# Kernel optimization log

Measured on AMD Instinct MI355X. Metric: run time of the kernel, lower is better.

## Reference

```python
import math
import jax, jax.numpy as jnp
import numpy as np

EMBED_DIM = 2048
NUM_HEADS = 16
NUM_KV_HEADS = 8
DEPTH = 12
HEAD_DIM = EMBED_DIM // NUM_HEADS // 2  # 64
N_REP = NUM_HEADS // NUM_KV_HEADS       # 2
SCALING = HEAD_DIM ** (-0.5)
LAMBDA_INIT = 0.8 - 0.6 * math.exp(-0.3 * DEPTH)
EPS = 1e-5


def _rope_cos_sin(seq_len, head_dim, offset=0):
    pos = jnp.arange(offset, offset + seq_len, dtype=jnp.float32)
    theta = jnp.arange(0, head_dim, 2, dtype=jnp.float32) / head_dim
    inv_freq = 1.0 / (10000.0 ** theta + 1e-8)
    sinusoid = pos[:, None] * inv_freq[None, :]  # [seq, head_dim//2]
    return jnp.cos(sinusoid), jnp.sin(sinusoid)


def _apply_rotary_interleaved(x, cos, sin):
    # x: [b, s, h, d]; cos/sin: [s, d//2]; interleaved pairs (even, odd)
    x1 = x[..., 0::2]
    x2 = x[..., 1::2]
    c = cos[None, :, None, :]
    s = sin[None, :, None, :]
    o1 = x1 * c - x2 * s
    o2 = x1 * s + x2 * c
    return jnp.stack([o1, o2], axis=-1).reshape(x.shape)


def setup_inputs() -> dict:
    key = jax.random.key(0)
    ks = jax.random.split(key, 12)
    d = EMBED_DIM
    inp = {
        "q": jax.random.normal(ks[0], (1, 2048, d), dtype=jnp.float32),
        "k": jax.random.normal(ks[1], (1, 2048, d), dtype=jnp.float32),
        "v": jax.random.normal(ks[2], (1, 2048, d), dtype=jnp.float32),
        "Wq": jax.random.normal(ks[3], (d, d), dtype=jnp.float32) * (d ** -0.5),
        "Wk": jax.random.normal(ks[4], (d, d // N_REP), dtype=jnp.float32) * (d ** -0.5),
        "Wv": jax.random.normal(ks[5], (d, d // N_REP), dtype=jnp.float32) * (d ** -0.5),
        "Wout": jax.random.normal(ks[6], (d, d), dtype=jnp.float32) * (d ** -0.5),
        "lq1": jax.random.normal(ks[7], (HEAD_DIM,), dtype=jnp.float32) * 0.1,
        "lk1": jax.random.normal(ks[8], (HEAD_DIM,), dtype=jnp.float32) * 0.1,
        "lq2": jax.random.normal(ks[9], (HEAD_DIM,), dtype=jnp.float32) * 0.1,
        "lk2": jax.random.normal(ks[10], (HEAD_DIM,), dtype=jnp.float32) * 0.1,
        "subln_w": jnp.ones((2 * HEAD_DIM,), dtype=jnp.float32),
    }
    return inp


def reference(q, k, v, Wq, Wk, Wv, Wout, lq1, lk1, lq2, lk2, subln_w):
    bsz, tgt_len, _ = q.shape
    src_len = k.shape[1]
    hd = HEAD_DIM

    qp = (q @ Wq).reshape(bsz, tgt_len, 2 * NUM_HEADS, hd)
    kp = (k @ Wk).reshape(bsz, src_len, 2 * NUM_KV_HEADS, hd)
    vp = (v @ Wv).reshape(bsz, src_len, NUM_KV_HEADS, 2 * hd)

    q_cos, q_sin = _rope_cos_sin(tgt_len, hd)
    k_cos, k_sin = _rope_cos_sin(src_len, hd)
    qp = _apply_rotary_interleaved(qp, q_cos, q_sin)
    kp = _apply_rotary_interleaved(kp, k_cos, k_sin)

    qp = jnp.transpose(qp, (0, 2, 1, 3)) * SCALING          # [b, 2H, t, hd]
    kp = jnp.repeat(jnp.transpose(kp, (0, 2, 1, 3)), N_REP, axis=1)  # [b, 2H, s, hd]
    vp = jnp.repeat(jnp.transpose(vp, (0, 2, 1, 3)), N_REP, axis=1)  # [b, H, s, 2hd]

    attn_weights = jnp.einsum('bhtd,bhsd->bhts', qp, kp)
    attn_weights = jax.nn.softmax(attn_weights.astype(jnp.float32), axis=-1).astype(qp.dtype)

    lambda_1 = jnp.exp(jnp.sum(lq1 * lk1))
    lambda_2 = jnp.exp(jnp.sum(lq2 * lk2))
    lambda_full = lambda_1 - lambda_2 + LAMBDA_INIT

    attn_weights = attn_weights.reshape(bsz, NUM_HEADS, 2, tgt_len, src_len)
    attn_weights = attn_weights[:, :, 0] - lambda_full * attn_weights[:, :, 1]

    attn = jnp.einsum('bhts,bhsd->bhtd', attn_weights, vp)  # [b, H, t, 2hd]

    # RMSNorm over last dim with affine weight
    rms = jax.lax.rsqrt(jnp.mean(jnp.square(attn), axis=-1, keepdims=True) + EPS)
    attn = attn * rms * subln_w
    attn = attn * (1.0 - LAMBDA_INIT)

    attn = jnp.transpose(attn, (0, 2, 1, 3)).reshape(bsz, tgt_len, NUM_HEADS * 2 * hd)
    return attn @ Wout
```

## Files before the change

### kernel.cpp

```cpp
#include <hip/hip_runtime.h>

typedef unsigned short u16;
typedef unsigned int u32;
typedef float f32x4 __attribute__((ext_vector_type(4)));
typedef __bf16 bf16x8 __attribute__((ext_vector_type(8)));
typedef __bf16 bf16x4 __attribute__((ext_vector_type(4)));

#define LAMBDA_INIT_F 0.7836057665316245f
#define ONE_MINUS_LI  0.2163942334683755f
#define THR_LOG2 11.0f
#define Q_SCALE 0.18033688011112042f

__device__ __forceinline__ u16 f2b(float f) {
  union { float f; u32 u; } x; x.f = f;
  u32 r = x.u + 0x7fffu + ((x.u >> 16) & 1u);
  return (u16)(r >> 16);
}

__device__ __forceinline__ f32x4 mfma16(bf16x8 a, bf16x8 b, f32x4 c) {
  return __builtin_amdgcn_mfma_f32_16x16x32_bf16(a, b, c, 0, 0, 0);
}

__device__ __forceinline__ float fexp2(float x) { return __builtin_amdgcn_exp2f(x); }

__device__ __forceinline__ void gll16(const void* gp, void* lp) {
  __builtin_amdgcn_global_load_lds((__attribute__((address_space(1))) void*)(gp),
                                   (__attribute__((address_space(3))) void*)(lp),
                                   16, 0, 0);
}

__global__ __launch_bounds__(256) void cast3_kernel(const float* __restrict__ q,
                                                    const float* __restrict__ k,
                                                    const float* __restrict__ v,
                                                    u16* __restrict__ qb,
                                                    u16* __restrict__ kb,
                                                    u16* __restrict__ vb) {
  int bid = blockIdx.x;
  int seg = bid >> 11;
  int i = (bid & 2047) * 256 + threadIdx.x;
  const float* in = seg == 0 ? q : (seg == 1 ? k : v);
  u16* out = seg == 0 ? qb : (seg == 1 ? kb : vb);
  const f32x4* p = (const f32x4*)(in + (size_t)i * 8);
  f32x4 a = p[0], b = p[1];
  union { u16 u[8]; f32x4 v; } o;
#pragma unroll
  for (int j = 0; j < 4; ++j) { o.u[j] = f2b(a[j]); o.u[4 + j] = f2b(b[j]); }
  *(f32x4*)(out + (size_t)i * 8) = o.v;
}

__device__ __forceinline__ void trans_body(const float* __restrict__ in,
                                           u16* __restrict__ out, int R, int C) {
  __shared__ float tile[32][33];
  int bx = blockIdx.x * 32;
  int by = blockIdx.y * 32;
  int tx = threadIdx.x & 31, ty = threadIdx.x >> 5;
#pragma unroll
  for (int i = 0; i < 32; i += 8)
    tile[ty + i][tx] = in[(size_t)(by + ty + i) * C + bx + tx];
  __syncthreads();
#pragma unroll
  for (int i = 0; i < 32; i += 8)
    out[(size_t)(bx + ty + i) * R + by + tx] = f2b(tile[tx][ty + i]);
}

__global__ __launch_bounds__(256) void wtrans_kernel(
    const float* __restrict__ Wq, u16* __restrict__ WqT,
    const float* __restrict__ Wk, u16* __restrict__ WkT,
    const float* __restrict__ Wv, u16* __restrict__ WvT,
    const float* __restrict__ Wo, u16* __restrict__ WoT) {
  int z = blockIdx.z;
  const float* in;
  u16* out;
  int C;
  if (z == 0)      { in = Wq; out = WqT; C = 2048; }
  else if (z == 1) { in = Wk; out = WkT; C = 1024; }
  else if (z == 2) { in = Wv; out = WvT; C = 1024; }
  else             { in = Wo; out = WoT; C = 2048; }
  if (blockIdx.x * 32 >= C) return;
  trans_body(in, out, 2048, C);
}

__global__ __launch_bounds__(256) void vtrans_kernel(const float* __restrict__ in,
                                                     u16* __restrict__ out) {
  __shared__ float tile[32][33];
  int bx = blockIdx.x * 32;
  int by = blockIdx.y * 32;
  int tx = threadIdx.x & 31, ty = threadIdx.x >> 5;
#pragma unroll
  for (int i = 0; i < 32; i += 8)
    tile[ty + i][tx] = in[(size_t)(by + ty + i) * 1024 + bx + tx];
  __syncthreads();
  int ptx = 8 * ((tx >> 2) & 3) + 4 * (tx >> 4) + (tx & 3);
#pragma unroll
  for (int i = 0; i < 32; i += 8)
    out[(size_t)(bx + ty + i) * 2048 + by + ptx] = f2b(tile[tx][ty + i]);
}

__global__ __launch_bounds__(256) void rope2_kernel(const float* __restrict__ QP,
                                                    const float* __restrict__ KP,
                                                    u16* __restrict__ Qh,
                                                    u16* __restrict__ Kh) {
  int hh = blockIdx.y;
  int idx = blockIdx.x * 256 + threadIdx.x;
  int j = idx & 31;
  int t = idx >> 5;
  const float* in;
  u16* out;
  int Hh, hl;
  float scale;
  if (hh < 32) { in = QP; out = Qh; Hh = 32; hl = hh; scale = Q_SCALE; }
  else         { in = KP; out = Kh; Hh = 16; hl = hh - 32; scale = 1.0f; }
  const float* src = in + (size_t)t * (Hh * 64) + hl * 64 + 2 * j;
  float x1 = src[0], x2 = src[1];
  float theta = (float)j * (1.0f / 32.0f);
  float denom = expf(theta * 9.210340371976184f);
  float invf = 1.0f / (denom + 1e-8f);
  float ang = (float)t * invf;
  float s = sinf(ang), c = cosf(ang);
  float o1 = (x1 * c - x2 * s) * scale;
  float o2 = (x1 * s + x2 * c) * scale;
  u32 pk = (u32)f2b(o1) | ((u32)f2b(o2) << 16);
  *(u32*)(out + ((size_t)hl * 2048 + t) * 64 + 2 * j) = pk;
}

__device__ __forceinline__ void gemm_body64(u16* As, u16* Bs,
                                            const u16* __restrict__ A,
                                            const u16* __restrict__ Bt,
                                            float* __restrict__ C,
                                            int N, int K, int bx, int by) {
  const int tid = threadIdx.x;
  const int lane = tid & 63;
  const int wave = tid >> 6;
  const int m0 = by * 128;
  const int n0 = bx * 64;
  const int wm = (wave >> 1) * 64;
  const int wn = (wave & 1) * 32;
  const int g = lane >> 4, c = lane & 15;

  f32x4 acc[4][2];
#pragma unroll
  for (int i = 0; i < 4; ++i)
#pragma unroll
    for (int j = 0; j < 2; ++j) acc[i][j] = (f32x4){0.f, 0.f, 0.f, 0.f};

  for (int k0 = 0; k0 < K; k0 += 64) {
    __syncthreads();
#pragma unroll
    for (int it = 0; it < 4; ++it) {
      int gi = it * 256 + tid;
      int R = gi >> 3;
      int lg = (gi & 7) ^ (R & 7);
      gll16(A + (size_t)(m0 + R) * K + k0 + lg * 8, As + gi * 8);
    }
#pragma unroll
    for (int it = 0; it < 2; ++it) {
      int gi = it * 256 + tid;
      int R = gi >> 3;
      int lg = (gi & 7) ^ (R & 7);
      gll16(Bt + (size_t)(n0 + R) * K + k0 + lg * 8, Bs + gi * 8);
    }
    __syncthreads();
#pragma unroll
    for (int kk = 0; kk < 2; ++kk) {
      bf16x8 af[4], bf[2];
      int ph = ((kk * 4 + g) ^ (c & 7)) * 8;
#pragma unroll
      for (int i = 0; i < 4; ++i) af[i] = *(const bf16x8*)&As[(wm + i * 16 + c) * 64 + ph];
#pragma unroll
      for (int j = 0; j < 2; ++j) bf[j] = *(const bf16x8*)&Bs[(wn + j * 16 + c) * 64 + ph];
#pragma unroll
      for (int i = 0; i < 4; ++i)
#pragma unroll
        for (int j = 0; j < 2; ++j) acc[i][j] = mfma16(af[i], bf[j], acc[i][j]);
    }
  }
#pragma unroll
  for (int i = 0; i < 4; ++i)
#pragma unroll
    for (int j = 0; j < 2; ++j) {
      int mrow = m0 + wm + i * 16 + g * 4;
      int ncol = n0 + wn + j * 16 + c;
#pragma unroll
      for (int r = 0; r < 4; ++r) C[(size_t)(mrow + r) * N + ncol] = acc[i][j][r];
    }
}

__global__ __launch_bounds__(256, 4) void gemm_qkv_kernel(
    const u16* __restrict__ qb, const u16* __restrict__ WqT, float* __restrict__ QP,
    const u16* __restrict__ kb, const u16* __restrict__ WkT, float* __restrict__ KP,
    const u16* __restrict__ vb, const u16* __restrict__ WvT, float* __restrict__ VP) {
  __shared__ u16 As[128 * 64];
  __shared__ u16 Bs[64 * 64];
  int bid = ((blockIdx.x & 7) << 7) | (blockIdx.x >> 3);
  if (bid < 512) {
    gemm_body64(As, Bs, qb, WqT, QP, 2048, 2048, bid & 31, bid >> 5);
  } else if (bid < 768) {
    int t = bid - 512;
    gemm_body64(As, Bs, kb, WkT, KP, 1024, 2048, t & 15, t >> 4);
  } else {
    int t = bid - 768;
    gemm_body64(As, Bs, vb, WvT, VP, 1024, 2048, t & 15, t >> 4);
  }
}

__global__ __launch_bounds__(256, 2) void gemm_one_kernel(const u16* __restrict__ A,
                                                          const u16* __restrict__ Bt,
                                                          float* __restrict__ C) {
  __shared__ u16 As[128 * 64];
  __shared__ u16 Bs[64 * 64];
  int bid = ((blockIdx.x & 7) << 6) | (blockIdx.x >> 3);
  gemm_body64(As, Bs, A, Bt, C, 2048, 2048, bid & 31, bid >> 5);
}

__global__ __launch_bounds__(512, 2) void attn_kernel(const u16* __restrict__ Qb,
                                                      const u16* __restrict__ Kb,
                                                      const u16* __restrict__ Vt,
                                                      u16* __restrict__ AO,
                                                      const float* __restrict__ lq1,
                                                      const float* __restrict__ lk1,
                                                      const float* __restrict__ lq2,
                                                      const float* __restrict__ lk2,
                                                      const float* __restrict__ subln) {
  const int b = ((blockIdx.x & 7) << 5) | (blockIdx.x >> 3);
  const int h = b >> 4;
  const int tid = threadIdx.x;
  const int wave = tid >> 6;
  const int lane = tid & 63;
  const int t0 = ((b & 15) * 8 + wave) * 16;
  const int g = lane >> 4, c = lane & 15;
  const int c7 = c & 7;

  __shared__ u16 smem[24576];

  const u16* Kh = Kb + (size_t)h * 2048 * 64;
  const u16* Vh = Vt + (size_t)(h >> 1) * 128 * 2048;

  float myl1 = lq1[lane] * lk1[lane];
  float myl2 = lq2[lane] * lk2[lane];
#pragma unroll
  for (int off = 32; off; off >>= 1) {
    myl1 += __shfl_xor(myl1, off);
    myl2 += __shfl_xor(myl2, off);
  }
  const float lambda_full = expf(myl1) - expf(myl2) + LAMBDA_INIT_F;

  bf16x8 qf[2][2];
#pragma unroll
  for (int e = 0; e < 2; ++e)
#pragma unroll
    for (int d = 0; d < 2; ++d)
      qf[e][d] = *(const bf16x8*)(Qb + ((size_t)(2 * h + e) * 2048 + t0 + c) * 64 + d * 32 + g * 8);

  const int kb0 = c * 64 + ((g ^ c7) * 8);
  const int kb1 = kb0 ^ 32;

  const u16* ksrc0;
  const u16* vsrc0;
  const u16* vsrc1;
  { int gi = tid;       int R = gi >> 3; ksrc0 = Kh + R * 64 + ((gi & 7) ^ (R & 7)) * 8; }
  { int gi = tid;       int R = gi >> 3; vsrc0 = Vh + (size_t)R * 2048 + ((gi & 7) ^ (R & 7)) * 8; }
  { int gi = 512 + tid; int R = gi >> 3; vsrc1 = Vh + (size_t)R * 2048 + ((gi & 7) ^ (R & 7)) * 8; }

  f32x4 O[2][8];
#pragma unroll
  for (int e = 0; e < 2; ++e)
#pragma unroll
    for (int f = 0; f < 8; ++f) O[e][f] = (f32x4){0.f, 0.f, 0.f, 0.f};
  float m0 = -1e30f, m1 = -1e30f, ls0 = 0.f, ls1 = 0.f;

#define STAGE(kOff, vOff, s0)                                   \
  do {                                                          \
    gll16(ksrc0 + (size_t)(s0) * 64, smem + (kOff) + tid * 8);  \
    gll16(vsrc0 + (s0), smem + (vOff) + tid * 8);               \
    gll16(vsrc1 + (s0), smem + (vOff) + 4096 + tid * 8);        \
  } while (0)

#define TILE(kOff, vOff)                                                      \
  do {                                                                        \
    bf16x8 kf[4][2];                                                          \
    _Pragma("unroll") for (int sf = 0; sf < 4; ++sf) {                        \
      kf[sf][0] = *(const bf16x8*)&smem[(kOff) + kb0 + sf * 1024];            \
      kf[sf][1] = *(const bf16x8*)&smem[(kOff) + kb1 + sf * 1024];            \
    }                                                                         \
    f32x4 sa[2][4];                                                           \
    _Pragma("unroll") for (int e = 0; e < 2; ++e)                             \
      _Pragma("unroll") for (int sf = 0; sf < 4; ++sf) {                      \
        f32x4 z = (f32x4){0.f, 0.f, 0.f, 0.f};                                \
        z = mfma16(kf[sf][0], qf[e][0], z);                                   \
        z = mfma16(kf[sf][1], qf[e][1], z);                                   \
        sa[e][sf] = z;                                                        \
      }                                                                       \
    bf16x8 vv0[8];                                                            \
    _Pragma("unroll") for (int f = 0; f < 8; ++f)                             \
      vv0[f] = *(const bf16x8*)&smem[(vOff) + kb0 + f * 1024];                \
    bf16x8 paf[2][2];                                                         \
    _Pragma("unroll") for (int e = 0; e < 2; ++e) {                           \
      float& m_e = e ? m1 : m0;                                               \
      float& ls_e = e ? ls1 : ls0;                                            \
      float mx = sa[e][0][0];                                                 \
      _Pragma("unroll") for (int sf = 0; sf < 4; ++sf)                        \
        _Pragma("unroll") for (int r = 0; r < 4; ++r)                         \
          mx = fmaxf(mx, sa[e][sf][r]);                                       \
      mx = fmaxf(mx, __shfl_xor(mx, 16));                                     \
      mx = fmaxf(mx, __shfl_xor(mx, 32));                                     \
      if (__any(mx > m_e + THR_LOG2)) {                                       \
        float mn = fmaxf(m_e, mx);                                            \
        float sc = fexp2(m_e - mn);                                           \
        m_e = mn;                                                             \
        ls_e *= sc;                                                           \
        float scr[4];                                                         \
        _Pragma("unroll") for (int r = 0; r < 4; ++r) scr[r] = __shfl(sc, g * 4 + r); \
        _Pragma("unroll") for (int ff = 0; ff < 8; ++ff)                      \
          _Pragma("unroll") for (int r = 0; r < 4; ++r) O[e][ff][r] *= scr[r]; \
      }                                                                       \
      float p[4][4];                                                          \
      float sum = 0.f;                                                        \
      _Pragma("unroll") for (int sf = 0; sf < 4; ++sf)                        \
        _Pragma("unroll") for (int r = 0; r < 4; ++r) {                       \
          float pv = fexp2(sa[e][sf][r] - m_e);                               \
          p[sf][r] = pv;                                                      \
          sum += pv;                                                          \
        }                                                                     \
      sum += __shfl_xor(sum, 16);                                             \
      sum += __shfl_xor(sum, 32);                                             \
      ls_e += sum;                                                            \
      paf[e][0] = (bf16x8){(__bf16)p[0][0], (__bf16)p[0][1], (__bf16)p[0][2], (__bf16)p[0][3], \
                           (__bf16)p[1][0], (__bf16)p[1][1], (__bf16)p[1][2], (__bf16)p[1][3]}; \
      paf[e][1] = (bf16x8){(__bf16)p[2][0], (__bf16)p[2][1], (__bf16)p[2][2], (__bf16)p[2][3], \
                           (__bf16)p[3][0], (__bf16)p[3][1], (__bf16)p[3][2], (__bf16)p[3][3]}; \
    }                                                                         \
    __builtin_amdgcn_s_setprio(1);                                            \
    bf16x8 vv1[8];                                                            \
    _Pragma("unroll") for (int f = 0; f < 8; ++f)                             \
      vv1[f] = *(const bf16x8*)&smem[(vOff) + kb1 + f * 1024];                \
    _Pragma("unroll") for (int f = 0; f < 8; ++f) {                           \
      O[0][f] = mfma16(paf[0][0], vv0[f], O[0][f]);                           \
      O[1][f] = mfma16(paf[1][0], vv0[f], O[1][f]);                           \
    }                                                                         \
    _Pragma("unroll") for (int f = 0; f < 8; ++f) {                           \
      O[0][f] = mfma16(paf[0][1], vv1[f], O[0][f]);                           \
      O[1][f] = mfma16(paf[1][1], vv1[f], O[1][f]);                           \
    }                                                                         \
    __builtin_amdgcn_s_setprio(0);                                            \
  } while (0)

  STAGE(0, 8192, 0);

#pragma unroll 1
  for (int t = 0; t < 32; t += 2) {
    __syncthreads();
    STAGE(4096, 16384, (t + 1) * 64);
    TILE(0, 8192);
    __syncthreads();
    if (t < 30) STAGE(0, 8192, (t + 2) * 64);
    TILE(4096, 16384);
  }

  float inv0 = 1.f / ls0, inv1 = 1.f / ls1;
  float i0[4], i1[4];
#pragma unroll
  for (int r = 0; r < 4; ++r) {
    i0[r] = __shfl(inv0, g * 4 + r);
    i1[r] = __shfl(inv1, g * 4 + r);
  }
  float res[8][4];
  float ss[4] = {0.f, 0.f, 0.f, 0.f};
#pragma unroll
  for (int f = 0; f < 8; ++f)
#pragma unroll
    for (int r = 0; r < 4; ++r) {
      float vv = O[0][f][r] * i0[r] - lambda_full * (O[1][f][r] * i1[r]);
      res[f][r] = vv;
      ss[r] += vv * vv;
    }
#pragma unroll
  for (int off = 1; off < 16; off <<= 1)
#pragma unroll
    for (int r = 0; r < 4; ++r) ss[r] += __shfl_xor(ss[r], off);
  float rms[4];
#pragma unroll
  for (int r = 0; r < 4; ++r)
    rms[r] = rsqrtf(ss[r] * (1.0f / 128.0f) + 1e-5f) * ONE_MINUS_LI;
  float w[8];
#pragma unroll
  for (int f = 0; f < 8; ++f) w[f] = subln[f * 16 + c];
#pragma unroll
  for (int f = 0; f < 8; ++f)
#pragma unroll
    for (int r = 0; r < 4; ++r)
      AO[(size_t)(t0 + g * 4 + r) * 2048 + h * 128 + f * 16 + c] = f2b(res[f][r] * rms[r] * w[f]);
}

extern "C" void kernel_launch(void* const* d_in, const int* in_sizes, int n_in,
                              void* d_out, int out_size, void* d_ws, size_t ws_size,
                              hipStream_t stream) {
  const float* q     = (const float*)d_in[0];
  const float* k     = (const float*)d_in[1];
  const float* v     = (const float*)d_in[2];
  const float* Wq    = (const float*)d_in[3];
  const float* Wk    = (const float*)d_in[4];
  const float* Wv    = (const float*)d_in[5];
  const float* Wout  = (const float*)d_in[6];
  const float* lq1   = (const float*)d_in[7];
  const float* lk1   = (const float*)d_in[8];
  const float* lq2   = (const float*)d_in[9];
  const float* lk2   = (const float*)d_in[10];
  const float* subln = (const float*)d_in[11];
  float* out = (float*)d_out;

  char* ws = (char*)d_ws;
  size_t off = 0;
  auto alloc = [&](size_t bytes) -> void* {
    void* p = ws + off;
    off += (bytes + 255) & ~(size_t)255;
    return p;
  };
  u16* qb  = (u16*)alloc(2048ull * 2048 * 2);
  u16* kb  = (u16*)alloc(2048ull * 2048 * 2);
  u16* vb  = (u16*)alloc(2048ull * 2048 * 2);
  u16* WqT = (u16*)alloc(2048ull * 2048 * 2);
  u16* WkT = (u16*)alloc(1024ull * 2048 * 2);
  u16* WvT = (u16*)alloc(1024ull * 2048 * 2);
  u16* WoT = (u16*)alloc(2048ull * 2048 * 2);
  float* QP = (float*)alloc(2048ull * 2048 * 4);
  float* KP = (float*)alloc(2048ull * 1024 * 4);
  float* VP = (float*)alloc(2048ull * 1024 * 4);
  u16* Qh  = (u16*)alloc(32ull * 2048 * 64 * 2);
  u16* Kh  = (u16*)alloc(16ull * 2048 * 64 * 2);
  u16* Vt  = (u16*)alloc(1024ull * 2048 * 2);
  u16* AO  = (u16*)QP;

  cast3_kernel<<<6144, 256, 0, stream>>>(q, k, v, qb, kb, vb);
  wtrans_kernel<<<dim3(64, 64, 4), 256, 0, stream>>>(Wq, WqT, Wk, WkT, Wv, WvT, Wout, WoT);
  gemm_qkv_kernel<<<1024, 256, 0, stream>>>(qb, WqT, QP, kb, WkT, KP, vb, WvT, VP);
  rope2_kernel<<<dim3(256, 48), 256, 0, stream>>>(QP, KP, Qh, Kh);
  vtrans_kernel<<<dim3(32, 64), 256, 0, stream>>>(VP, Vt);
  attn_kernel<<<256, 512, 0, stream>>>(Qh, Kh, Vt, AO, lq1, lk1, lq2, lk2, subln);
  gemm_one_kernel<<<512, 256, 0, stream>>>(AO, WoT, out);
}
```

Before: 166.8 us.

## Fuse RoPE and V transpose into QKV GEMM epilogue, enlarge GEMM tiles

The QKV projection GEMM now writes bf16 head-major Q/K with rotary embedding applied, and transposed V, directly from its epilogue. This removes the fp32 QP/KP/VP intermediates and the separate rope and V-transpose kernels. A cos/sin table is computed in extra blocks of the cast kernel. GEMM tiles grow from 128x64 to 128x128, which doubles per-wave accumulators and halves the block count. That could lower occupancy and leave fewer blocks to spread across CUs.

```diff
diff --git a/kernel.cpp b/kernel.cpp
--- a/kernel.cpp
+++ b/kernel.cpp
@@ -3,6 +3,8 @@
 typedef unsigned short u16;
 typedef unsigned int u32;
 typedef float f32x4 __attribute__((ext_vector_type(4)));
+typedef float f32x2 __attribute__((ext_vector_type(2)));
+typedef unsigned int u32x2 __attribute__((ext_vector_type(2)));
 typedef __bf16 bf16x8 __attribute__((ext_vector_type(8)));
 typedef __bf16 bf16x4 __attribute__((ext_vector_type(4)));
 
@@ -34,8 +36,19 @@
                                                     const float* __restrict__ v,
                                                     u16* __restrict__ qb,
                                                     u16* __restrict__ kb,
-                                                    u16* __restrict__ vb) {
+                                                    u16* __restrict__ vb,
+                                                    f32x2* __restrict__ tbl) {
   int bid = blockIdx.x;
+  if (bid >= 6144) {
+    int idx = (bid - 6144) * 256 + threadIdx.x;
+    int t = idx >> 5, j = idx & 31;
+    float theta = (float)j * (1.0f / 32.0f);
+    float denom = expf(theta * 9.210340371976184f);
+    float invf = 1.0f / (denom + 1e-8f);
+    float ang = (float)t * invf;
+    tbl[idx] = (f32x2){cosf(ang), sinf(ang)};
+    return;
+  }
   int seg = bid >> 11;
   int i = (bid & 2047) * 256 + threadIdx.x;
   const float* in = seg == 0 ? q : (seg == 1 ? k : v);
@@ -80,68 +93,28 @@
   trans_body(in, out, 2048, C);
 }
 
-__global__ __launch_bounds__(256) void vtrans_kernel(const float* __restrict__ in,
-                                                     u16* __restrict__ out) {
-  __shared__ float tile[32][33];
-  int bx = blockIdx.x * 32;
-  int by = blockIdx.y * 32;
-  int tx = threadIdx.x & 31, ty = threadIdx.x >> 5;
-#pragma unroll
-  for (int i = 0; i < 32; i += 8)
-    tile[ty + i][tx] = in[(size_t)(by + ty + i) * 1024 + bx + tx];
-  __syncthreads();
-  int ptx = 8 * ((tx >> 2) & 3) + 4 * (tx >> 4) + (tx & 3);
-#pragma unroll
-  for (int i = 0; i < 32; i += 8)
-    out[(size_t)(bx + ty + i) * 2048 + by + ptx] = f2b(tile[tx][ty + i]);
-}
-
-__global__ __launch_bounds__(256) void rope2_kernel(const float* __restrict__ QP,
-                                                    const float* __restrict__ KP,
-                                                    u16* __restrict__ Qh,
-                                                    u16* __restrict__ Kh) {
-  int hh = blockIdx.y;
-  int idx = blockIdx.x * 256 + threadIdx.x;
-  int j = idx & 31;
-  int t = idx >> 5;
-  const float* in;
-  u16* out;
-  int Hh, hl;
-  float scale;
-  if (hh < 32) { in = QP; out = Qh; Hh = 32; hl = hh; scale = Q_SCALE; }
-  else         { in = KP; out = Kh; Hh = 16; hl = hh - 32; scale = 1.0f; }
-  const float* src = in + (size_t)t * (Hh * 64) + hl * 64 + 2 * j;
-  float x1 = src[0], x2 = src[1];
-  float theta = (float)j * (1.0f / 32.0f);
-  float denom = expf(theta * 9.210340371976184f);
-  float invf = 1.0f / (denom + 1e-8f);
-  float ang = (float)t * invf;
-  float s = sinf(ang), c = cosf(ang);
-  float o1 = (x1 * c - x2 * s) * scale;
-  float o2 = (x1 * s + x2 * c) * scale;
-  u32 pk = (u32)f2b(o1) | ((u32)f2b(o2) << 16);
-  *(u32*)(out + ((size_t)hl * 2048 + t) * 64 + 2 * j) = pk;
-}
-
-__device__ __forceinline__ void gemm_body64(u16* As, u16* Bs,
-                                            const u16* __restrict__ A,
-                                            const u16* __restrict__ Bt,
-                                            float* __restrict__ C,
-                                            int N, int K, int bx, int by) {
+template <int MODE>
+__device__ __forceinline__ void gemm_body(u16* As, u16* Bs,
+                                          const u16* __restrict__ A,
+                                          const u16* __restrict__ Bt,
+                                          void* __restrict__ Cout,
+                                          const f32x2* __restrict__ tbl,
+                                          float scale,
+                                          int N, int K, int bx, int by) {
   const int tid = threadIdx.x;
   const int lane = tid & 63;
   const int wave = tid >> 6;
   const int m0 = by * 128;
-  const int n0 = bx * 64;
+  const int n0 = bx * 128;
   const int wm = (wave >> 1) * 64;
-  const int wn = (wave & 1) * 32;
+  const int wn = (wave & 1) * 64;
   const int g = lane >> 4, c = lane & 15;
 
-  f32x4 acc[4][2];
+  f32x4 acc[4][4];
 #pragma unroll
   for (int i = 0; i < 4; ++i)
 #pragma unroll
-    for (int j = 0; j < 2; ++j) acc[i][j] = (f32x4){0.f, 0.f, 0.f, 0.f};
+    for (int j = 0; j < 4; ++j) acc[i][j] = (f32x4){0.f, 0.f, 0.f, 0.f};
 
   for (int k0 = 0; k0 < K; k0 += 64) {
     __syncthreads();
@@ -151,55 +124,96 @@
       int R = gi >> 3;
       int lg = (gi & 7) ^ (R & 7);
       gll16(A + (size_t)(m0 + R) * K + k0 + lg * 8, As + gi * 8);
-    }
-#pragma unroll
-    for (int it = 0; it < 2; ++it) {
-      int gi = it * 256 + tid;
-      int R = gi >> 3;
-      int lg = (gi & 7) ^ (R & 7);
       gll16(Bt + (size_t)(n0 + R) * K + k0 + lg * 8, Bs + gi * 8);
     }
     __syncthreads();
 #pragma unroll
     for (int kk = 0; kk < 2; ++kk) {
-      bf16x8 af[4], bf[2];
-      int ph = ((kk * 4 + g) ^ (c & 7)) * 8;
-#pragma unroll
-      for (int i = 0; i < 4; ++i) af[i] = *(const bf16x8*)&As[(wm + i * 16 + c) * 64 + ph];
-#pragma unroll
-      for (int j = 0; j < 2; ++j) bf[j] = *(const bf16x8*)&Bs[(wn + j * 16 + c) * 64 + ph];
+      bf16x8 af[4], bf[4];
+#pragma unroll
+      for (int i = 0; i < 4; ++i) {
+        int ph = ((kk * 4 + g) ^ (c & 7)) * 8;
+        af[i] = *(const bf16x8*)&As[(wm + i * 16 + c) * 64 + ph];
+        bf[i] = *(const bf16x8*)&Bs[(wn + i * 16 + c) * 64 + ph];
+      }
 #pragma unroll
       for (int i = 0; i < 4; ++i)
 #pragma unroll
-        for (int j = 0; j < 2; ++j) acc[i][j] = mfma16(af[i], bf[j], acc[i][j]);
+        for (int j = 0; j < 4; ++j) acc[i][j] = mfma16(af[i], bf[j], acc[i][j]);
     }
   }
-#pragma unroll
-  for (int i = 0; i < 4; ++i)
-#pragma unroll
-    for (int j = 0; j < 2; ++j) {
-      int mrow = m0 + wm + i * 16 + g * 4;
-      int ncol = n0 + wn + j * 16 + c;
-#pragma unroll
-      for (int r = 0; r < 4; ++r) C[(size_t)(mrow + r) * N + ncol] = acc[i][j][r];
-    }
-}
-
-__global__ __launch_bounds__(256, 4) void gemm_qkv_kernel(
-    const u16* __restrict__ qb, const u16* __restrict__ WqT, float* __restrict__ QP,
-    const u16* __restrict__ kb, const u16* __restrict__ WkT, float* __restrict__ KP,
-    const u16* __restrict__ vb, const u16* __restrict__ WvT, float* __restrict__ VP) {
+
+  if constexpr (MODE == 0) {
+    float* C = (float*)Cout;
+#pragma unroll
+    for (int i = 0; i < 4; ++i)
+#pragma unroll
+      for (int j = 0; j < 4; ++j) {
+        int mrow = m0 + wm + i * 16 + g * 4;
+        int ncol = n0 + wn + j * 16 + c;
+#pragma unroll
+        for (int r = 0; r < 4; ++r) C[(size_t)(mrow + r) * N + ncol] = acc[i][j][r];
+      }
+  } else if constexpr (MODE == 1) {
+    u16* Oh = (u16*)Cout;
+    const bool even = (c & 1) == 0;
+#pragma unroll
+    for (int i = 0; i < 4; ++i)
+#pragma unroll
+      for (int j = 0; j < 4; ++j) {
+        int mrow = m0 + wm + i * 16 + g * 4;
+        int ncol = n0 + wn + j * 16 + c;
+        int hh = ncol >> 6;
+        int d = ncol & 63;
+        int jd = d >> 1;
+        f32x4 own = acc[i][j];
+        f32x4 part;
+#pragma unroll
+        for (int r = 0; r < 4; ++r) part[r] = __shfl_xor(own[r], 1);
+        if (even) {
+#pragma unroll
+          for (int r = 0; r < 4; ++r) {
+            f32x2 cs = tbl[(mrow + r) * 32 + jd];
+            float o1 = (own[r] * cs[0] - part[r] * cs[1]) * scale;
+            float o2 = (own[r] * cs[1] + part[r] * cs[0]) * scale;
+            u32 pk = (u32)f2b(o1) | ((u32)f2b(o2) << 16);
+            *(u32*)&Oh[((size_t)hh * 2048 + mrow + r) * 64 + d] = pk;
+          }
+        }
+      }
+  } else {
+    u16* Vt = (u16*)Cout;
+#pragma unroll
+    for (int i = 0; i < 4; ++i)
+#pragma unroll
+      for (int j = 0; j < 4; ++j) {
+        int ncol = n0 + wn + j * 16 + c;
+        int tblk = (m0 + wm + i * 16) >> 5;
+        int p0 = 8 * g + 4 * (i & 1);
+        u32x2 pk;
+        pk[0] = (u32)f2b(acc[i][j][0]) | ((u32)f2b(acc[i][j][1]) << 16);
+        pk[1] = (u32)f2b(acc[i][j][2]) | ((u32)f2b(acc[i][j][3]) << 16);
+        *(u32x2*)&Vt[(size_t)ncol * 2048 + tblk * 32 + p0] = pk;
+      }
+  }
+}
+
+__global__ __launch_bounds__(256, 2) void gemm_qkv_kernel(
+    const u16* __restrict__ qb, const u16* __restrict__ WqT, u16* __restrict__ Qh,
+    const u16* __restrict__ kb, const u16* __restrict__ WkT, u16* __restrict__ Kh,
+    const u16* __restrict__ vb, const u16* __restrict__ WvT, u16* __restrict__ Vt,
+    const f32x2* __restrict__ tbl) {
   __shared__ u16 As[128 * 64];
-  __shared__ u16 Bs[64 * 64];
-  int bid = ((blockIdx.x & 7) << 7) | (blockIdx.x >> 3);
-  if (bid < 512) {
-    gemm_body64(As, Bs, qb, WqT, QP, 2048, 2048, bid & 31, bid >> 5);
-  } else if (bid < 768) {
-    int t = bid - 512;
-    gemm_body64(As, Bs, kb, WkT, KP, 1024, 2048, t & 15, t >> 4);
+  __shared__ u16 Bs[128 * 64];
+  int bid = ((blockIdx.x & 7) << 6) | (blockIdx.x >> 3);
+  if (bid < 256) {
+    gemm_body<1>(As, Bs, qb, WqT, Qh, tbl, Q_SCALE, 2048, 2048, bid & 15, bid >> 4);
+  } else if (bid < 384) {
+    int t = bid - 256;
+    gemm_body<1>(As, Bs, kb, WkT, Kh, tbl, 1.0f, 1024, 2048, t & 7, t >> 3);
   } else {
-    int t = bid - 768;
-    gemm_body64(As, Bs, vb, WvT, VP, 1024, 2048, t & 15, t >> 4);
+    int t = bid - 384;
+    gemm_body<2>(As, Bs, vb, WvT, Vt, tbl, 1.0f, 1024, 2048, t & 7, t >> 3);
   }
 }
 
@@ -207,9 +221,9 @@
                                                           const u16* __restrict__ Bt,
                                                           float* __restrict__ C) {
   __shared__ u16 As[128 * 64];
-  __shared__ u16 Bs[64 * 64];
-  int bid = ((blockIdx.x & 7) << 6) | (blockIdx.x >> 3);
-  gemm_body64(As, Bs, A, Bt, C, 2048, 2048, bid & 31, bid >> 5);
+  __shared__ u16 Bs[128 * 64];
+  int bid = ((blockIdx.x & 7) << 5) | (blockIdx.x >> 3);
+  gemm_body<0>(As, Bs, A, Bt, C, nullptr, 1.0f, 2048, 2048, bid & 15, bid >> 4);
 }
 
 __global__ __launch_bounds__(512, 2) void attn_kernel(const u16* __restrict__ Qb,
@@ -422,19 +436,15 @@
   u16* WkT = (u16*)alloc(1024ull * 2048 * 2);
   u16* WvT = (u16*)alloc(1024ull * 2048 * 2);
   u16* WoT = (u16*)alloc(2048ull * 2048 * 2);
-  float* QP = (float*)alloc(2048ull * 2048 * 4);
-  float* KP = (float*)alloc(2048ull * 1024 * 4);
-  float* VP = (float*)alloc(2048ull * 1024 * 4);
+  f32x2* tbl = (f32x2*)alloc(2048ull * 32 * 8);
   u16* Qh  = (u16*)alloc(32ull * 2048 * 64 * 2);
   u16* Kh  = (u16*)alloc(16ull * 2048 * 64 * 2);
   u16* Vt  = (u16*)alloc(1024ull * 2048 * 2);
-  u16* AO  = (u16*)QP;
-
-  cast3_kernel<<<6144, 256, 0, stream>>>(q, k, v, qb, kb, vb);
+  u16* AO  = (u16*)alloc(2048ull * 2048 * 2);
+
+  cast3_kernel<<<6400, 256, 0, stream>>>(q, k, v, qb, kb, vb, tbl);
   wtrans_kernel<<<dim3(64, 64, 4), 256, 0, stream>>>(Wq, WqT, Wk, WkT, Wv, WvT, Wout, WoT);
-  gemm_qkv_kernel<<<1024, 256, 0, stream>>>(qb, WqT, QP, kb, WkT, KP, vb, WvT, VP);
-  rope2_kernel<<<dim3(256, 48), 256, 0, stream>>>(QP, KP, Qh, Kh);
-  vtrans_kernel<<<dim3(32, 64), 256, 0, stream>>>(VP, Vt);
+  gemm_qkv_kernel<<<512, 256, 0, stream>>>(qb, WqT, Qh, kb, WkT, Kh, vb, WvT, Vt, tbl);
   attn_kernel<<<256, 512, 0, stream>>>(Qh, Kh, Vt, AO, lq1, lk1, lq2, lk2, subln);
-  gemm_one_kernel<<<512, 256, 0, stream>>>(AO, WoT, out);
-}
+  gemm_one_kernel<<<256, 256, 0, stream>>>(AO, WoT, out);
+}
```

Result: faster. 156.2 us (-6.3%).
